# Optimization experiments

Measured on AMD Instinct MI355X. Metric: run time of the kernel, lower is better.

The kernel has to match this reference:

```python
import jax, jax.numpy as jnp
import numpy as np

B, S, E, H, L = 4, 1024, 1024, 16, 4
D = E // H
MAX_POS = 1024
NI, NS = 10000, 1000
W_SCALE = 0.02


def setup_inputs() -> dict:
    key = jax.random.key(0)
    ks = jax.random.split(key, 24)
    r = lambda k, sh: jax.random.normal(k, sh, dtype=jnp.float32) * W_SCALE
    return {
        'item_inputs': jax.random.randint(ks[0], (B, S), 0, NI),
        'skill_inputs': jax.random.randint(ks[1], (B, S), 0, NS),
        'label_inputs': jax.random.randint(ks[2], (B, S), 0, 2),
        'item_ids': jax.random.randint(ks[3], (B, S), 0, NI),
        'skill_ids': jax.random.randint(ks[4], (B, S), 0, NS),
        'emb_item': r(ks[5], (NI, E)),
        'emb_skill': r(ks[6], (NS, E)),
        'W_in': r(ks[7], (E, 2 * E)),
        'b_in': r(ks[8], (E,)),
        'Wq': r(ks[9], (L, E, E)),
        'bq': r(ks[10], (L, E)),
        'Wk': r(ks[11], (L, E, E)),
        'bk': r(ks[12], (L, E)),
        'Wv': r(ks[13], (L, E, E)),
        'bv': r(ks[14], (L, E)),
        'Wg': r(ks[15], (L, H, E)),
        'bg': r(ks[16], (L, H)),
        'pos_key': r(ks[17], (L, MAX_POS, D)),
        'Wl': r(ks[18], (L, 3, E, E)),
        'bl': r(ks[19], (L, 3, E)),
        'W_out': r(ks[20], (1, E)),
        'b_out': r(ks[21], (1,)),
    }


def _forward(item_inputs, skill_inputs, emb_item, emb_skill, W_in, b_in,
             Wq, bq, Wk, bk, Wv, bv, Wg, bg, pos_key, Wl, bl, W_out, b_out):
    # input embedding: concat(item, skill) -> linear
    x = jnp.concatenate([emb_item[item_inputs], emb_skill[skill_inputs]], axis=-1)
    x = x @ W_in.T + b_in  # [B, S, E]
    pos_ids = jnp.clip(jnp.arange(S), 0, MAX_POS - 1)
    inv_sqrt_d = 1.0 / np.sqrt(D).astype(np.float32)
    for l in range(L):
        # NOTE (faithful to source): k and v are computed from q0 = linear_q(x)
        q0 = x @ Wq[l].T + bq[l]
        k = q0 @ Wk[l].T + bk[l]
        v = q0 @ Wv[l].T + bv[l]
        # global bias: [B, S, H] -> [B, H, S, 1] (broadcast over key dim)
        glo = jnp.transpose(k @ Wg[l].T + bg[l], (0, 2, 1))[..., None]
        qh = q0.reshape(B, S, H, D).transpose(0, 2, 1, 3)  # [B,H,S,D]
        kh = k.reshape(B, S, H, D).transpose(0, 2, 1, 3)
        vh = v.reshape(B, S, H, D).transpose(0, 2, 1, 3)
        pe = pos_key[l][pos_ids]  # [S, D]
        scores = (jnp.einsum('bhqd,bhkd->bhqk', qh, kh)
                  + glo
                  + jnp.einsum('bhqd,kd->bhqk', qh, pe)) * inv_sqrt_d
        prob = jax.nn.softmax(scores, axis=-1)
        o = jnp.einsum('bhqk,bhkd->bhqd', prob, vh)
        o = o.transpose(0, 2, 1, 3).reshape(B, S, E)
        for i in range(3):  # GELU MLP stack
            o = jax.nn.gelu(o @ Wl[l, i].T + bl[l, i], approximate=False)
        x = o
    out = x @ W_out.T + b_out  # [B, S, 1]
    return out[..., 0]


def reference(item_inputs, skill_inputs, label_inputs, item_ids, skill_ids,
              emb_item, emb_skill, W_in, b_in, Wq, bq, Wk, bk, Wv, bv,
              Wg, bg, pos_key, Wl, bl, W_out, b_out):
    return _forward(item_inputs, skill_inputs, emb_item, emb_skill, W_in, b_in,
                    Wq, bq, Wk, bk, Wv, bv, Wg, bg, pos_key, Wl, bl, W_out, b_out)
```

## Files before the change

kernel.cpp:

```cpp
#include <hip/hip_runtime.h>
#include <hip/hip_bf16.h>


#define B_ 4
#define S_ 1024
#define E_ 1024
#define H_ 16
#define D_ 64
#define L_ 4
#define M_ (B_ * S_)
#define EE (E_ * E_)

typedef __attribute__((ext_vector_type(8))) __bf16 bf16x8;
typedef __attribute__((ext_vector_type(4))) __bf16 bf16x4;
typedef __attribute__((ext_vector_type(4))) float f32x4;
typedef __attribute__((ext_vector_type(8))) unsigned short u16x8;

__device__ __forceinline__ float bf2f(unsigned short u) {
    union { unsigned int i; float f; } x;
    x.i = ((unsigned int)u) << 16;
    return x.f;
}
__device__ __forceinline__ float gelu_exact(float x) {
    return 0.5f * x * (1.0f + erff(x * 0.70710678118654752f));
}
__device__ __forceinline__ bf16x8 pack8(const float4 a, const float4 b) {
    bf16x8 o;
    o[0] = (__bf16)a.x; o[1] = (__bf16)a.y; o[2] = (__bf16)a.z; o[3] = (__bf16)a.w;
    o[4] = (__bf16)b.x; o[5] = (__bf16)b.y; o[6] = (__bf16)b.z; o[7] = (__bf16)b.w;
    return o;
}

__device__ __forceinline__ size_t kpack_idx(int m, int col) {
    const int b = m >> 10, srow = m & (S_ - 1);
    const int h = col >> 6, d = col & 63;
    const int bh = b * H_ + h;
    const int kt = srow >> 6, kb = (srow >> 4) & 3, l15 = srow & 15;
    const int kc = d >> 5, lhi = (d >> 3) & 3, j = d & 7;
    const int frag = ((bh * 16 + kt) * 4 + kb) * 2 + kc;
    return (size_t)frag * 512 + (size_t)(lhi * 16 + l15) * 8 + j;
}
__device__ __forceinline__ size_t vpack_idx(int m, int col) {
    const int b = m >> 10, key = m & (S_ - 1);
    const int h = col >> 6, d = col & 63;
    const int bh = b * H_ + h;
    const int kt = key >> 6;
    const int k6 = key & 63;
    const int kc = k6 >> 5, kl = k6 & 31;
    const int lhi = (kl >> 2) & 3;
    const int j = ((kl >> 4) << 2) | (kl & 3);
    const int db = d >> 4, l15 = d & 15;
    const int frag = ((bh * 16 + kt) * 4 + db) * 2 + kc;
    return (size_t)frag * 512 + (size_t)(lhi * 16 + l15) * 8 + j;
}

__global__ __launch_bounds__(256) void cvt_all_weights(
    const float* __restrict__ Wq, const float* __restrict__ Wk,
    const float* __restrict__ Wv, const float* __restrict__ Wl,
    const float* __restrict__ Win, __bf16* __restrict__ out) {
    const int y = blockIdx.y;
    const int off = (blockIdx.x * 256 + threadIdx.x) * 16;
    const float* src;
    if (y >= 24) {
        src = Win + (size_t)(y - 24) * EE + off;
    } else {
        const int l = y / 6, mat = y - l * 6;
        src = (mat == 0) ? Wq + (size_t)l * EE + off
            : (mat == 1) ? Wk + (size_t)l * EE + off
            : (mat == 2) ? Wv + (size_t)l * EE + off
                         : Wl + ((size_t)l * 3 + (mat - 3)) * EE + off;
    }
    __bf16* dst = out + (size_t)y * EE + off;
#pragma unroll
    for (int h = 0; h < 2; ++h) {
        const float4 a = *(const float4*)(src + h * 8);
        const float4 b = *(const float4*)(src + h * 8 + 4);
        *(bf16x8*)(dst + h * 8) = pack8(a, b);
    }
}

__global__ __launch_bounds__(256) void embed_gather(
    const int* __restrict__ item_idx, const int* __restrict__ skill_idx,
    const float* __restrict__ emb_item, const float* __restrict__ emb_skill,
    __bf16* __restrict__ Xc) {
    const int r = blockIdx.x;
    const int c = threadIdx.x * 8;
    const float* s = (c < E_) ? emb_item + (size_t)item_idx[r] * E_ + c
                              : emb_skill + (size_t)skill_idx[r] * E_ + (c - E_);
    const float4 a = *(const float4*)s;
    const float4 b = *(const float4*)(s + 4);
    *(bf16x8*)(Xc + (size_t)r * 2048 + c) = pack8(a, b);
}

template <int ACT, int PACK>
__global__ __launch_bounds__(256) void gemm64(
    const __bf16* __restrict__ A, const __bf16* __restrict__ Bm,
    const float* __restrict__ bias, __bf16* __restrict__ C, int K,
    const float* __restrict__ pe) {
    __shared__ __bf16 As[64 * 128];
    __shared__ __bf16 Bs[64 * 128];
    const int tid = threadIdx.x;
    const int lane = tid & 63;
    const int wid = tid >> 6;
    const int wm = wid >> 1;
    const int wn = wid & 1;
    const int l15 = lane & 15, lhi = lane >> 4;

    const int gx = gridDim.x;
    const int id = blockIdx.y * gx + blockIdx.x;
    const int nwg = gx * gridDim.y;
    const int swz = (id & 7) * (nwg >> 3) + (id >> 3);
    const int m0 = (swz / gx) * 64;
    const int n0 = (swz % gx) * 64;

    const __bf16* pa[4];
    __bf16* la[4];
    const __bf16* pb[4];
    __bf16* lb[4];
#pragma unroll
    for (int j = 0; j < 4; ++j) {
        const int c = wid * 256 + j * 64 + lane;
        const int row = c >> 4, ch = c & 15;
        pa[j] = A + (size_t)(m0 + row) * K + ((ch ^ (row & 15)) << 3);
        la[j] = As + (size_t)c * 8;
        pb[j] = Bm + (size_t)(n0 + row) * K + ((ch ^ (row & 15)) << 3);
        lb[j] = Bs + (size_t)c * 8;
    }

    int aoff[2][4], boff[2][4];
#pragma unroll
    for (int mi = 0; mi < 2; ++mi) {
        const int row = wm * 32 + mi * 16 + l15;
#pragma unroll
        for (int kc = 0; kc < 4; ++kc)
            aoff[mi][kc] = row * 128 + (((kc * 4 + lhi) ^ (row & 15)) << 3);
    }
#pragma unroll
    for (int ni = 0; ni < 2; ++ni) {
        const int row = wn * 32 + ni * 16 + l15;
#pragma unroll
        for (int kc = 0; kc < 4; ++kc)
            boff[ni][kc] = row * 128 + (((kc * 4 + lhi) ^ (row & 15)) << 3);
    }

    f32x4 acc[2][2] = {};

    for (int k0 = 0; k0 < K; k0 += 128) {
#pragma unroll
        for (int j = 0; j < 4; ++j) {
            __builtin_amdgcn_global_load_lds(
                (const __attribute__((address_space(1))) unsigned int*)(pa[j] + k0),
                (__attribute__((address_space(3))) unsigned int*)la[j], 16, 0, 0);
            __builtin_amdgcn_global_load_lds(
                (const __attribute__((address_space(1))) unsigned int*)(pb[j] + k0),
                (__attribute__((address_space(3))) unsigned int*)lb[j], 16, 0, 0);
        }
        __syncthreads();
        bf16x8 af[2][4], bfr[2][4];
#pragma unroll
        for (int mi = 0; mi < 2; ++mi)
#pragma unroll
            for (int kc = 0; kc < 4; ++kc)
                af[mi][kc] = *(const bf16x8*)(As + aoff[mi][kc]);
#pragma unroll
        for (int ni = 0; ni < 2; ++ni)
#pragma unroll
            for (int kc = 0; kc < 4; ++kc)
                bfr[ni][kc] = *(const bf16x8*)(Bs + boff[ni][kc]);
#pragma unroll
        for (int mi = 0; mi < 2; ++mi)
#pragma unroll
            for (int ni = 0; ni < 2; ++ni)
#pragma unroll
                for (int kc = 0; kc < 4; ++kc)
                    acc[mi][ni] = __builtin_amdgcn_mfma_f32_16x16x32_bf16(
                        af[mi][kc], bfr[ni][kc], acc[mi][ni], 0, 0, 0);
        __syncthreads();
    }

    const int ccol0 = n0 + wn * 32 + l15;
    const int crow0 = m0 + wm * 32 + (lhi << 2);
#pragma unroll
    for (int mi = 0; mi < 2; ++mi) {
#pragma unroll
        for (int ni = 0; ni < 2; ++ni) {
            const int col = ccol0 + ni * 16;
            const float bsum = bias[col];
#pragma unroll
            for (int r = 0; r < 4; ++r) {
                const int row = crow0 + mi * 16 + r;
                float v = acc[mi][ni][r] + bsum;
                if (PACK == 0) {
                    if (ACT) v = gelu_exact(v);
                    C[(size_t)row * E_ + col] = (__bf16)v;
                } else if (PACK == 1) {
                    v += pe[((row & (S_ - 1)) << 6) + (col & (D_ - 1))];
                    C[kpack_idx(row, col)] = (__bf16)v;
                } else {
                    C[vpack_idx(row, col)] = (__bf16)v;
                }
            }
        }
    }
}

__global__ __launch_bounds__(512) void attn_mfma(
    const __bf16* __restrict__ Q, const __bf16* __restrict__ Kp,
    const __bf16* __restrict__ Vp, __bf16* __restrict__ O) {
    __shared__ __bf16 Slds[2][2][8 * 512];
    const int tid = threadIdx.x;
    const int lane = tid & 63;
    const int w = tid >> 6;
    const int l15 = lane & 15, lhi = lane >> 4;

    const int id = blockIdx.y * gridDim.x + blockIdx.x;
    const int swz = (id & 7) * 64 + (id >> 3);
    const int q0 = (swz & 7) * 128 + w * 16;
    const int bh = swz >> 3;
    const int bb = bh >> 4, hh = bh & 15;

    bf16x8 qf[2];
    {
        const __bf16* qrow =
            Q + (size_t)(bb * S_ + q0 + l15) * E_ + hh * 64 + lhi * 8;
#pragma unroll
        for (int kc = 0; kc < 2; ++kc) {
            const u16x8 raw = *(const u16x8*)(qrow + kc * 32);
            bf16x8 v;
#pragma unroll
            for (int j = 0; j < 8; ++j) v[j] = (__bf16)(bf2f(raw[j]) * 0.125f);
            qf[kc] = v;
        }
    }

    const __bf16* kpw = Kp + ((size_t)bh * 16 * 8 + w) * 512 + lane * 8;
    const __bf16* vpw = Vp + ((size_t)bh * 16 * 8 + w) * 512 + lane * 8;

    float m_l = -1e30f, l_l = 0.f;
    f32x4 oacc[4] = {};

    __builtin_amdgcn_global_load_lds(
        (const __attribute__((address_space(1))) unsigned int*)(kpw),
        (__attribute__((address_space(3))) unsigned int*)(&Slds[0][0][w * 512]),
        16, 0, 0);
    __builtin_amdgcn_global_load_lds(
        (const __attribute__((address_space(1))) unsigned int*)(vpw),
        (__attribute__((address_space(3))) unsigned int*)(&Slds[0][1][w * 512]),
        16, 0, 0);

#pragma unroll 2
    for (int kt = 0; kt < S_ / 64; ++kt) {
        const int cur = kt & 1;
        __syncthreads();
        if (kt < S_ / 64 - 1) {
            const size_t fo = (size_t)(kt + 1) * 8 * 512;
            __builtin_amdgcn_global_load_lds(
                (const __attribute__((address_space(1))) unsigned int*)(kpw + fo),
                (__attribute__((address_space(3))) unsigned int*)(
                    &Slds[cur ^ 1][0][w * 512]), 16, 0, 0);
            __builtin_amdgcn_global_load_lds(
                (const __attribute__((address_space(1))) unsigned int*)(vpw + fo),
                (__attribute__((address_space(3))) unsigned int*)(
                    &Slds[cur ^ 1][1][w * 512]), 16, 0, 0);
        }
        const __bf16* kl = &Slds[cur][0][0];
        const __bf16* vl = &Slds[cur][1][0];
        f32x4 s[4];
#pragma unroll
        for (int kb = 0; kb < 4; ++kb) {
            const bf16x8 k0 = *(const bf16x8*)(kl + (kb * 2 + 0) * 512 + lane * 8);
            const bf16x8 k1 = *(const bf16x8*)(kl + (kb * 2 + 1) * 512 + lane * 8);
            f32x4 z = {};
            z = __builtin_amdgcn_mfma_f32_16x16x32_bf16(k0, qf[0], z, 0, 0, 0);
            s[kb] = __builtin_amdgcn_mfma_f32_16x16x32_bf16(k1, qf[1], z, 0, 0, 0);
        }
        float mx0 = fmaxf(fmaxf(s[0][0], s[0][1]), fmaxf(s[0][2], s[0][3]));
        float mx1 = fmaxf(fmaxf(s[1][0], s[1][1]), fmaxf(s[1][2], s[1][3]));
        float mx2 = fmaxf(fmaxf(s[2][0], s[2][1]), fmaxf(s[2][2], s[2][3]));
        float mx3 = fmaxf(fmaxf(s[3][0], s[3][1]), fmaxf(s[3][2], s[3][3]));
        float mx = fmaxf(fmaxf(mx0, mx1), fmaxf(mx2, mx3));
        mx = fmaxf(mx, __shfl_xor(mx, 16));
        mx = fmaxf(mx, __shfl_xor(mx, 32));
        const float mnew = fmaxf(m_l, mx);
        const float corr = __expf(m_l - mnew);
        float p[4][4];
        float rs = 0.f;
#pragma unroll
        for (int kb = 0; kb < 4; ++kb) {
            float sb = 0.f;
#pragma unroll
            for (int r = 0; r < 4; ++r) {
                p[kb][r] = __expf(s[kb][r] - mnew);
                sb += p[kb][r];
            }
            rs += sb;
        }
        rs += __shfl_xor(rs, 16);
        rs += __shfl_xor(rs, 32);
        l_l = l_l * corr + rs;
        m_l = mnew;
#pragma unroll
        for (int db = 0; db < 4; ++db)
#pragma unroll
            for (int r = 0; r < 4; ++r) oacc[db][r] *= corr;
        bf16x8 pf[2];
#pragma unroll
        for (int kc = 0; kc < 2; ++kc) {
            bf16x8 v;
#pragma unroll
            for (int r = 0; r < 4; ++r) {
                v[r] = (__bf16)p[kc * 2][r];
                v[r + 4] = (__bf16)p[kc * 2 + 1][r];
            }
            pf[kc] = v;
        }
#pragma unroll
        for (int db = 0; db < 4; ++db) {
            const bf16x8 v0 = *(const bf16x8*)(vl + (db * 2 + 0) * 512 + lane * 8);
            const bf16x8 v1 = *(const bf16x8*)(vl + (db * 2 + 1) * 512 + lane * 8);
            oacc[db] = __builtin_amdgcn_mfma_f32_16x16x32_bf16(v0, pf[0], oacc[db], 0, 0, 0);
            oacc[db] = __builtin_amdgcn_mfma_f32_16x16x32_bf16(v1, pf[1], oacc[db], 0, 0, 0);
        }
    }
    const float inv_l = 1.f / l_l;
    __bf16* orow = O + (size_t)(bb * S_ + q0 + l15) * E_ + hh * 64 + lhi * 4;
#pragma unroll
    for (int db = 0; db < 4; ++db) {
        bf16x4 ov;
#pragma unroll
        for (int r = 0; r < 4; ++r) ov[r] = (__bf16)(oacc[db][r] * inv_l);
        *(bf16x4*)(orow + db * 16) = ov;
    }
}

__global__ __launch_bounds__(256) void final_proj(
    const __bf16* __restrict__ X, const float* __restrict__ Wout,
    const float* __restrict__ bout, float* __restrict__ out) {
    const int wid = threadIdx.x >> 6, lane = threadIdx.x & 63;
    const int m = blockIdx.x * 4 + wid;
    const __bf16* xrow = X + (size_t)m * E_;
    float acc = 0.f;
#pragma unroll
    for (int c = 0; c < 2; ++c) {
        const int idx = c * 512 + lane * 8;
        const u16x8 xv = *(const u16x8*)(xrow + idx);
        const float4 w1 = *(const float4*)(Wout + idx);
        const float4 w2 = *(const float4*)(Wout + idx + 4);
        acc += bf2f(xv[0]) * w1.x + bf2f(xv[1]) * w1.y + bf2f(xv[2]) * w1.z +
               bf2f(xv[3]) * w1.w + bf2f(xv[4]) * w2.x + bf2f(xv[5]) * w2.y +
               bf2f(xv[6]) * w2.z + bf2f(xv[7]) * w2.w;
    }
#pragma unroll
    for (int off = 32; off; off >>= 1) acc += __shfl_xor(acc, off, 64);
    if (lane == 0) out[m] = acc + bout[0];
}

extern "C" void kernel_launch(void* const* d_in, const int* in_sizes, int n_in,
                              void* d_out, int out_size, void* d_ws, size_t ws_size,
                              hipStream_t stream) {
    const int* item_inputs = (const int*)d_in[0];
    const int* skill_inputs = (const int*)d_in[1];
    const float* emb_item = (const float*)d_in[5];
    const float* emb_skill = (const float*)d_in[6];
    const float* W_in = (const float*)d_in[7];
    const float* b_in = (const float*)d_in[8];
    const float* Wq = (const float*)d_in[9];
    const float* bq = (const float*)d_in[10];
    const float* Wk = (const float*)d_in[11];
    const float* bk = (const float*)d_in[12];
    const float* Wv = (const float*)d_in[13];
    const float* bv = (const float*)d_in[14];
    const float* pos_key = (const float*)d_in[17];
    const float* Wl = (const float*)d_in[18];
    const float* bl = (const float*)d_in[19];
    const float* W_out = (const float*)d_in[20];
    const float* b_out = (const float*)d_in[21];
    float* out = (float*)d_out;

    const size_t SZ = (size_t)M_ * E_;
    __bf16* Xc = (__bf16*)d_ws;
    __bf16* X = Xc + (size_t)M_ * 2048;
    __bf16* Qb = X + SZ;
    __bf16* Kp = Qb + SZ;
    __bf16* Vp = Kp + SZ;
    __bf16* Wall = Vp + SZ;

    const dim3 gg64(16, 64);
    const dim3 bb(256);

    embed_gather<<<dim3(M_), bb, 0, stream>>>(item_inputs, skill_inputs,
                                              emb_item, emb_skill, Xc);
    cvt_all_weights<<<dim3(EE / 4096, 26), bb, 0, stream>>>(Wq, Wk, Wv, Wl,
                                                            W_in, Wall);

    gemm64<0, 0><<<gg64, bb, 0, stream>>>(Xc, Wall + 24 * (size_t)EE, b_in, X,
                                          2048, nullptr);

    for (int l = 0; l < L_; ++l) {
        __bf16* Wbuf = Wall + (size_t)l * 6 * EE;
        const float* pe_l = pos_key + (size_t)l * S_ * D_;
        gemm64<0, 0><<<gg64, bb, 0, stream>>>(X, Wbuf + 0 * EE, bq + l * E_, Qb, E_, nullptr);
        gemm64<0, 1><<<gg64, bb, 0, stream>>>(Qb, Wbuf + 1 * EE, bk + l * E_, Kp, E_, pe_l);
        gemm64<0, 2><<<gg64, bb, 0, stream>>>(Qb, Wbuf + 2 * EE, bv + l * E_, Vp, E_, nullptr);
        attn_mfma<<<dim3(S_ / 128, B_ * H_), dim3(512), 0, stream>>>(Qb, Kp, Vp, X);
        gemm64<1, 0><<<gg64, bb, 0, stream>>>(X, Wbuf + 3 * EE, bl + (l * 3 + 0) * E_, Qb, E_, nullptr);
        gemm64<1, 0><<<gg64, bb, 0, stream>>>(Qb, Wbuf + 4 * EE, bl + (l * 3 + 1) * E_, Kp, E_, nullptr);
        gemm64<1, 0><<<gg64, bb, 0, stream>>>(Kp, Wbuf + 5 * EE, bl + (l * 3 + 2) * E_, X, E_, nullptr);
    }
    final_proj<<<dim3(M_ / 4), bb, 0, stream>>>(X, W_out, b_out, out);
}
```

Measured before the change: 545.9 us.

## Process 128-key tiles per attention iteration and widen weight conversion per thread

```diff
diff --git a/kernel.cpp b/kernel.cpp
--- a/kernel.cpp
+++ b/kernel.cpp
@@ -59,7 +59,7 @@
     const float* __restrict__ Wv, const float* __restrict__ Wl,
     const float* __restrict__ Win, __bf16* __restrict__ out) {
     const int y = blockIdx.y;
-    const int off = (blockIdx.x * 256 + threadIdx.x) * 16;
+    const int off = (blockIdx.x * 256 + threadIdx.x) * 32;
     const float* src;
     if (y >= 24) {
         src = Win + (size_t)(y - 24) * EE + off;
@@ -71,12 +71,15 @@
                          : Wl + ((size_t)l * 3 + (mat - 3)) * EE + off;
     }
     __bf16* dst = out + (size_t)y * EE + off;
-#pragma unroll
-    for (int h = 0; h < 2; ++h) {
-        const float4 a = *(const float4*)(src + h * 8);
-        const float4 b = *(const float4*)(src + h * 8 + 4);
-        *(bf16x8*)(dst + h * 8) = pack8(a, b);
-    }
+    float4 a[4], b[4];
+#pragma unroll
+    for (int h = 0; h < 4; ++h) {
+        a[h] = *(const float4*)(src + h * 8);
+        b[h] = *(const float4*)(src + h * 8 + 4);
+    }
+#pragma unroll
+    for (int h = 0; h < 4; ++h)
+        *(bf16x8*)(dst + h * 8) = pack8(a[h], b[h]);
 }
 
 __global__ __launch_bounds__(256) void embed_gather(
@@ -207,7 +210,7 @@
 __global__ __launch_bounds__(512) void attn_mfma(
     const __bf16* __restrict__ Q, const __bf16* __restrict__ Kp,
     const __bf16* __restrict__ Vp, __bf16* __restrict__ O) {
-    __shared__ __bf16 Slds[2][2][8 * 512];
+    __shared__ __bf16 Slds[2][2][16 * 512];
     const int tid = threadIdx.x;
     const int lane = tid & 63;
     const int w = tid >> 6;
@@ -233,60 +236,69 @@
         }
     }
 
-    const __bf16* kpw = Kp + ((size_t)bh * 16 * 8 + w) * 512 + lane * 8;
-    const __bf16* vpw = Vp + ((size_t)bh * 16 * 8 + w) * 512 + lane * 8;
+    const __bf16* kpw = Kp + ((size_t)bh * 16 * 8 + w * 2) * 512 + lane * 8;
+    const __bf16* vpw = Vp + ((size_t)bh * 16 * 8 + w * 2) * 512 + lane * 8;
 
     float m_l = -1e30f, l_l = 0.f;
     f32x4 oacc[4] = {};
 
-    __builtin_amdgcn_global_load_lds(
-        (const __attribute__((address_space(1))) unsigned int*)(kpw),
-        (__attribute__((address_space(3))) unsigned int*)(&Slds[0][0][w * 512]),
-        16, 0, 0);
-    __builtin_amdgcn_global_load_lds(
-        (const __attribute__((address_space(1))) unsigned int*)(vpw),
-        (__attribute__((address_space(3))) unsigned int*)(&Slds[0][1][w * 512]),
-        16, 0, 0);
-
-#pragma unroll 2
-    for (int kt = 0; kt < S_ / 64; ++kt) {
-        const int cur = kt & 1;
+#pragma unroll
+    for (int f = 0; f < 2; ++f) {
+        __builtin_amdgcn_global_load_lds(
+            (const __attribute__((address_space(1))) unsigned int*)(kpw + f * 512),
+            (__attribute__((address_space(3))) unsigned int*)(
+                &Slds[0][0][(w * 2 + f) * 512]), 16, 0, 0);
+        __builtin_amdgcn_global_load_lds(
+            (const __attribute__((address_space(1))) unsigned int*)(vpw + f * 512),
+            (__attribute__((address_space(3))) unsigned int*)(
+                &Slds[0][1][(w * 2 + f) * 512]), 16, 0, 0);
+    }
+
+    for (int t = 0; t < S_ / 128; ++t) {
+        const int cur = t & 1;
         __syncthreads();
-        if (kt < S_ / 64 - 1) {
-            const size_t fo = (size_t)(kt + 1) * 8 * 512;
-            __builtin_amdgcn_global_load_lds(
-                (const __attribute__((address_space(1))) unsigned int*)(kpw + fo),
-                (__attribute__((address_space(3))) unsigned int*)(
-                    &Slds[cur ^ 1][0][w * 512]), 16, 0, 0);
-            __builtin_amdgcn_global_load_lds(
-                (const __attribute__((address_space(1))) unsigned int*)(vpw + fo),
-                (__attribute__((address_space(3))) unsigned int*)(
-                    &Slds[cur ^ 1][1][w * 512]), 16, 0, 0);
+        if (t < S_ / 128 - 1) {
+            const size_t fo = (size_t)(t + 1) * 16 * 512;
+#pragma unroll
+            for (int f = 0; f < 2; ++f) {
+                __builtin_amdgcn_global_load_lds(
+                    (const __attribute__((address_space(1))) unsigned int*)(
+                        kpw + fo + f * 512),
+                    (__attribute__((address_space(3))) unsigned int*)(
+                        &Slds[cur ^ 1][0][(w * 2 + f) * 512]), 16, 0, 0);
+                __builtin_amdgcn_global_load_lds(
+                    (const __attribute__((address_space(1))) unsigned int*)(
+                        vpw + fo + f * 512),
+                    (__attribute__((address_space(3))) unsigned int*)(
+                        &Slds[cur ^ 1][1][(w * 2 + f) * 512]), 16, 0, 0);
+            }
         }
         const __bf16* kl = &Slds[cur][0][0];
         const __bf16* vl = &Slds[cur][1][0];
-        f32x4 s[4];
-#pragma unroll
-        for (int kb = 0; kb < 4; ++kb) {
-            const bf16x8 k0 = *(const bf16x8*)(kl + (kb * 2 + 0) * 512 + lane * 8);
-            const bf16x8 k1 = *(const bf16x8*)(kl + (kb * 2 + 1) * 512 + lane * 8);
+        f32x4 s[8];
+#pragma unroll
+        for (int kb = 0; kb < 8; ++kb) {
+            const int fb = ((kb >> 2) * 8 + (kb & 3) * 2);
+            const bf16x8 k0 = *(const bf16x8*)(kl + (fb + 0) * 512 + lane * 8);
+            const bf16x8 k1 = *(const bf16x8*)(kl + (fb + 1) * 512 + lane * 8);
             f32x4 z = {};
             z = __builtin_amdgcn_mfma_f32_16x16x32_bf16(k0, qf[0], z, 0, 0, 0);
             s[kb] = __builtin_amdgcn_mfma_f32_16x16x32_bf16(k1, qf[1], z, 0, 0, 0);
         }
-        float mx0 = fmaxf(fmaxf(s[0][0], s[0][1]), fmaxf(s[0][2], s[0][3]));
-        float mx1 = fmaxf(fmaxf(s[1][0], s[1][1]), fmaxf(s[1][2], s[1][3]));
-        float mx2 = fmaxf(fmaxf(s[2][0], s[2][1]), fmaxf(s[2][2], s[2][3]));
-        float mx3 = fmaxf(fmaxf(s[3][0], s[3][1]), fmaxf(s[3][2], s[3][3]));
-        float mx = fmaxf(fmaxf(mx0, mx1), fmaxf(mx2, mx3));
+        float mx = fmaxf(fmaxf(s[0][0], s[0][1]), fmaxf(s[0][2], s[0][3]));
+#pragma unroll
+        for (int kb = 1; kb < 8; ++kb) {
+            mx = fmaxf(mx, fmaxf(fmaxf(s[kb][0], s[kb][1]),
+                                 fmaxf(s[kb][2], s[kb][3])));
+        }
         mx = fmaxf(mx, __shfl_xor(mx, 16));
         mx = fmaxf(mx, __shfl_xor(mx, 32));
         const float mnew = fmaxf(m_l, mx);
         const float corr = __expf(m_l - mnew);
-        float p[4][4];
+        float p[8][4];
         float rs = 0.f;
 #pragma unroll
-        for (int kb = 0; kb < 4; ++kb) {
+        for (int kb = 0; kb < 8; ++kb) {
             float sb = 0.f;
 #pragma unroll
             for (int r = 0; r < 4; ++r) {
@@ -303,23 +315,26 @@
         for (int db = 0; db < 4; ++db)
 #pragma unroll
             for (int r = 0; r < 4; ++r) oacc[db][r] *= corr;
-        bf16x8 pf[2];
-#pragma unroll
-        for (int kc = 0; kc < 2; ++kc) {
+        bf16x8 pf[4];
+#pragma unroll
+        for (int kcc = 0; kcc < 4; ++kcc) {
             bf16x8 v;
 #pragma unroll
             for (int r = 0; r < 4; ++r) {
-                v[r] = (__bf16)p[kc * 2][r];
-                v[r + 4] = (__bf16)p[kc * 2 + 1][r];
+                v[r] = (__bf16)p[kcc * 2][r];
+                v[r + 4] = (__bf16)p[kcc * 2 + 1][r];
             }
-            pf[kc] = v;
+            pf[kcc] = v;
         }
 #pragma unroll
         for (int db = 0; db < 4; ++db) {
-            const bf16x8 v0 = *(const bf16x8*)(vl + (db * 2 + 0) * 512 + lane * 8);
-            const bf16x8 v1 = *(const bf16x8*)(vl + (db * 2 + 1) * 512 + lane * 8);
-            oacc[db] = __builtin_amdgcn_mfma_f32_16x16x32_bf16(v0, pf[0], oacc[db], 0, 0, 0);
-            oacc[db] = __builtin_amdgcn_mfma_f32_16x16x32_bf16(v1, pf[1], oacc[db], 0, 0, 0);
+#pragma unroll
+            for (int kcc = 0; kcc < 4; ++kcc) {
+                const bf16x8 vv = *(const bf16x8*)(
+                    vl + (((kcc >> 1) * 8 + db * 2 + (kcc & 1))) * 512 + lane * 8);
+                oacc[db] = __builtin_amdgcn_mfma_f32_16x16x32_bf16(
+                    vv, pf[kcc], oacc[db], 0, 0, 0);
+            }
         }
     }
     const float inv_l = 1.f / l_l;
@@ -390,7 +405,7 @@
 
     embed_gather<<<dim3(M_), bb, 0, stream>>>(item_inputs, skill_inputs,
                                               emb_item, emb_skill, Xc);
-    cvt_all_weights<<<dim3(EE / 4096, 26), bb, 0, stream>>>(Wq, Wk, Wv, Wl,
+    cvt_all_weights<<<dim3(EE / 8192, 26), bb, 0, stream>>>(Wq, Wk, Wv, Wl,
                                                             W_in, Wall);
 
     gemm64<0, 0><<<gg64, bb, 0, stream>>>(Xc, Wall + 24 * (size_t)EE, b_in, X,
```

Measured after the change: 558.8 us. 1.02x slower.
